# Optimization experiments

Hardware: AMD Instinct MI355X
Metric: run time of the kernel (lower is better)

## Reference

```python
import jax, jax.numpy as jnp
import numpy as np

N_NODES = 50000
N_EDGES = 800000
IN_DIM = 64
H_DIM = 64


def setup_inputs() -> dict:
    key = jax.random.key(0)
    ks = jax.random.split(key, 6)
    feat = jax.random.normal(ks[0], (N_NODES, IN_DIM), dtype=jnp.float32)
    W1 = jax.random.normal(ks[1], (IN_DIM, H_DIM), dtype=jnp.float32) * (1.0 / np.sqrt(IN_DIM))
    b1 = jnp.zeros((H_DIM,), dtype=jnp.float32)
    W2 = jax.random.normal(ks[2], (H_DIM, 1), dtype=jnp.float32) * (1.0 / np.sqrt(H_DIM))
    b2 = jnp.zeros((1,), dtype=jnp.float32)
    src = jax.random.randint(ks[3], (N_EDGES,), 0, N_NODES, dtype=jnp.int32)
    dst = jax.random.randint(ks[4], (N_EDGES,), 0, N_NODES, dtype=jnp.int32)
    return {"feat": feat, "W1": W1, "b1": b1, "W2": W2, "b2": b2, "src": src, "dst": dst}


def _norms(src, dst, n_nodes):
    # DGL GraphConv norm='both': symmetric D^{-1/2} A D^{-1/2}, degrees clamped to >=1
    ones = jnp.ones(src.shape[0], dtype=jnp.float32)
    out_deg = jax.ops.segment_sum(ones, src, num_segments=n_nodes)
    in_deg = jax.ops.segment_sum(ones, dst, num_segments=n_nodes)
    out_norm = jax.lax.rsqrt(jnp.clip(out_deg, 1.0))
    in_norm = jax.lax.rsqrt(jnp.clip(in_deg, 1.0))
    return out_norm, in_norm


def _graph_conv(feat, W, b, src, dst, out_norm, in_norm, act):
    h = feat * out_norm[:, None]          # scale source features by D_out^{-1/2}
    msg = h[src]                          # gather along edges [E, d]
    agg = jax.ops.segment_sum(msg, dst, num_segments=feat.shape[0])  # scatter-sum to dst
    agg = agg * in_norm[:, None]          # scale by D_in^{-1/2}
    return act(agg @ W + b)


def reference(feat, W1, b1, W2, b2, src, dst):
    out_norm, in_norm = _norms(src, dst, feat.shape[0])
    h = _graph_conv(feat, W1, b1, src, dst, out_norm, in_norm, jax.nn.relu)
    return _graph_conv(h, W2, b2, src, dst, out_norm, in_norm, jax.nn.sigmoid)
```

## Files before the change

kernel.cpp:

```cpp
#include <hip/hip_runtime.h>
#include <hip/hip_fp16.h>
#include <math.h>


#define BS 256
#define EPB 2048
#define SCB 2048

__global__ __launch_bounds__(256, 4)
void histA_featw1_kernel(const int* __restrict__ src, const int* __restrict__ dst,
                         const float* __restrict__ feat, const float* __restrict__ W1,
                         int* __restrict__ dhist,
                         __half* __restrict__ featp,
                         int E, int N, int NB, int T, int M) {
    __shared__ float4 ftile[64 * 16];
    __shared__ int histD[256];
    __shared__ int histS[256];
    int tid = threadIdx.x;
    if ((int)blockIdx.x < T) {
        histD[tid] = 0; histS[tid] = 0;
        __syncthreads();
        int base = blockIdx.x * EPB;
        #pragma unroll
        for (int it = 0; it < EPB / BS; it++) {
            int e = base + it * BS + tid;
            if (e < E) {
                atomicAdd(&histD[dst[e] >> 8], 1);
                atomicAdd(&histS[src[e] >> 8], 1);
            }
        }
        __syncthreads();
        if (tid < NB) {
            dhist[tid * T + (int)blockIdx.x] = histD[tid];
            dhist[M + tid * T + (int)blockIdx.x] = histS[tid];
        }
    } else {
        int lane = tid & 63;
        int wave = tid >> 6;
        #define WD(i) float wv##i = W1[(i) * 64 + lane];
        WD(0)  WD(1)  WD(2)  WD(3)  WD(4)  WD(5)  WD(6)  WD(7)
        WD(8)  WD(9)  WD(10) WD(11) WD(12) WD(13) WD(14) WD(15)
        WD(16) WD(17) WD(18) WD(19) WD(20) WD(21) WD(22) WD(23)
        WD(24) WD(25) WD(26) WD(27) WD(28) WD(29) WD(30) WD(31)
        WD(32) WD(33) WD(34) WD(35) WD(36) WD(37) WD(38) WD(39)
        WD(40) WD(41) WD(42) WD(43) WD(44) WD(45) WD(46) WD(47)
        WD(48) WD(49) WD(50) WD(51) WD(52) WD(53) WD(54) WD(55)
        WD(56) WD(57) WD(58) WD(59) WD(60) WD(61) WD(62) WD(63)
        #undef WD
        int rBase = ((int)blockIdx.x - T) * 64;
        const float4* feat4 = (const float4*)feat;
        int maxF4 = N * 16 - 1;
        #pragma unroll
        for (int it = 0; it < 4; it++) {
            int idx = it * BS + tid;
            ftile[idx] = feat4[min(rBase * 16 + idx, maxF4)];
        }
        __syncthreads();
        #pragma unroll 1
        for (int rr = 0; rr < 16; rr++) {
            int r = wave * 16 + rr;
            const float4* ft = &ftile[r * 16];
            float a0 = 0.0f, a1 = 0.0f, a2 = 0.0f, a3 = 0.0f;
            #define RK(k4, wA, wB, wC, wD_) { float4 f = ft[k4]; \
                a0 = fmaf(f.x, wA, a0); a1 = fmaf(f.y, wB, a1); \
                a2 = fmaf(f.z, wC, a2); a3 = fmaf(f.w, wD_, a3); }
            RK(0,  wv0,  wv1,  wv2,  wv3)  RK(1,  wv4,  wv5,  wv6,  wv7)
            RK(2,  wv8,  wv9,  wv10, wv11) RK(3,  wv12, wv13, wv14, wv15)
            RK(4,  wv16, wv17, wv18, wv19) RK(5,  wv20, wv21, wv22, wv23)
            RK(6,  wv24, wv25, wv26, wv27) RK(7,  wv28, wv29, wv30, wv31)
            RK(8,  wv32, wv33, wv34, wv35) RK(9,  wv36, wv37, wv38, wv39)
            RK(10, wv40, wv41, wv42, wv43) RK(11, wv44, wv45, wv46, wv47)
            RK(12, wv48, wv49, wv50, wv51) RK(13, wv52, wv53, wv54, wv55)
            RK(14, wv56, wv57, wv58, wv59) RK(15, wv60, wv61, wv62, wv63)
            #undef RK
            int rowg = rBase + r;
            if (rowg < N)
                featp[(size_t)rowg * 64 + lane] = __float2half((a0 + a1) + (a2 + a3));
        }
    }
}

__global__ void scan1_kernel(const int* __restrict__ dhist, int* __restrict__ bsum, int M2) {
    __shared__ int s[256];
    int t = threadIdx.x;
    int base = blockIdx.x * SCB + t * 8;
    int sum = 0;
    #pragma unroll
    for (int i = 0; i < 8; i++) {
        int k = base + i;
        if (k < M2) sum += dhist[k];
    }
    s[t] = sum; __syncthreads();
    for (int off = 1; off < 256; off <<= 1) {
        int u = (t >= off) ? s[t - off] : 0; __syncthreads();
        s[t] += u; __syncthreads();
    }
    if (t == 255) bsum[blockIdx.x] = s[255];
}

__global__ void scan2_kernel(int* __restrict__ bsum, int NSB) {
    __shared__ int s[256];
    int t = threadIdx.x;
    int v = (t < NSB) ? bsum[t] : 0;
    s[t] = v; __syncthreads();
    for (int off = 1; off < 256; off <<= 1) {
        int u = (t >= off) ? s[t - off] : 0; __syncthreads();
        s[t] += u; __syncthreads();
    }
    if (t < NSB) bsum[t] = s[t] - v;
}

__global__ void scan3_kernel(int* __restrict__ dhist, const int* __restrict__ bsum, int M2) {
    __shared__ int s[256];
    int t = threadIdx.x;
    int base = blockIdx.x * SCB + t * 8;
    int v[8];
    int sum = 0;
    #pragma unroll
    for (int i = 0; i < 8; i++) {
        int k = base + i;
        v[i] = (k < M2) ? dhist[k] : 0;
        sum += v[i];
    }
    s[t] = sum; __syncthreads();
    for (int off = 1; off < 256; off <<= 1) {
        int u = (t >= off) ? s[t - off] : 0; __syncthreads();
        s[t] += u; __syncthreads();
    }
    int run = bsum[blockIdx.x] + s[t] - sum;
    #pragma unroll
    for (int i = 0; i < 8; i++) {
        int k = base + i;
        if (k < M2) dhist[k] = run;
        run += v[i];
    }
}

__global__ void partition_kernel(const int* __restrict__ src, const int* __restrict__ dst,
                                 const int* __restrict__ dhist,
                                 int* __restrict__ packed, unsigned char* __restrict__ srcPartB,
                                 int E, int NB, int T, int M) {
    __shared__ int darr[256];
    __shared__ int sarr[256];
    int tid = threadIdx.x;
    int b = blockIdx.x;
    darr[tid] = (tid < NB) ? dhist[tid * T + b] : 0;
    sarr[tid] = (tid < NB) ? (dhist[M + tid * T + b] - E) : 0;
    __syncthreads();
    int base = b * EPB;
    #pragma unroll
    for (int it = 0; it < EPB / BS; it++) {
        int e = base + it * BS + tid;
        if (e < E) {
            int d = dst[e], s2 = src[e];
            int pos = atomicAdd(&darr[d >> 8], 1);
            packed[pos] = s2 | ((d & 255) << 17);
            int pos2 = atomicAdd(&sarr[s2 >> 8], 1);
            srcPartB[pos2] = (unsigned char)(s2 & 255);
        }
    }
}

__global__ void finalize_kernel(const int* __restrict__ dhist,
                                const int* __restrict__ packed,
                                const unsigned char* __restrict__ srcPartB,
                                int* __restrict__ csr_src, int* __restrict__ in_deg,
                                int* __restrict__ row_start, int* __restrict__ out_deg,
                                __half* __restrict__ featp,
                                int N, int NB, int T, int M, int E) {
    __shared__ int hist[256];
    __shared__ int sc[256];
    int tid = threadIdx.x;
    int b = blockIdx.x;
    if (b < NB) {
        int lo = dhist[b * T];
        int hi = (b + 1 < NB) ? dhist[(b + 1) * T] : E;
        hist[tid] = 0; __syncthreads();
        for (int i = lo + tid; i < hi; i += BS)
            atomicAdd(&hist[(packed[i] >> 17) & 255], 1);
        __syncthreads();
        int v = hist[tid];
        sc[tid] = v; __syncthreads();
        for (int off = 1; off < 256; off <<= 1) {
            int u = (tid >= off) ? sc[tid - off] : 0; __syncthreads();
            sc[tid] += u; __syncthreads();
        }
        int ex = sc[tid] - v;
        int n = b * 256 + tid;
        if (n < N) { in_deg[n] = v; row_start[n] = lo + ex; }
        sc[tid] = lo + ex;
        __syncthreads();
        for (int i = lo + tid; i < hi; i += BS) {
            int pv = packed[i];
            int pos = atomicAdd(&sc[(pv >> 17) & 255], 1);
            csr_src[pos] = pv & 0x1FFFF;
        }
    } else {
        int sb = b - NB;
        int lo = dhist[M + sb * T] - E;
        int hi = ((sb + 1 < NB) ? dhist[M + (sb + 1) * T] : 2 * E) - E;
        hist[tid] = 0; __syncthreads();
        for (int i = lo + tid; i < hi; i += BS)
            atomicAdd(&hist[srcPartB[i]], 1);
        __syncthreads();
        int n = sb * 256 + tid;
        int od = hist[tid];
        if (n < N) out_deg[n] = od;
        float* snorm = (float*)sc;
        snorm[tid] = rsqrtf(fmaxf((float)od, 1.0f));
        __syncthreads();
        int nodes = min(256, N - sb * 256);
        uint4* fp = (uint4*)(featp + (size_t)sb * 256 * 64);
        int total = nodes * 8;
        for (int i = tid; i < total; i += BS) {
            float s = snorm[i >> 3];
            uint4 u = fp[i];
            __half2* hh = (__half2*)&u;
            #pragma unroll
            for (int c = 0; c < 4; c++) {
                float2 p = __half22float2(hh[c]);
                p.x *= s; p.y *= s;
                hh[c] = __float22half2_rn(p);
            }
            fp[i] = u;
        }
    }
}

__global__ void csr_agg1_kernel(const int* __restrict__ row_start, const int* __restrict__ in_deg,
                                const int* __restrict__ csr_src, const int* __restrict__ out_deg,
                                const __half* __restrict__ featp,
                                const float* __restrict__ b1, const float* __restrict__ W2,
                                float* __restrict__ s_buf, int N) {
    int gid = blockIdx.x * blockDim.x + threadIdx.x;
    int n = gid >> 6;
    if (n >= N) return;
    int lane = threadIdx.x & 63;
    int g = lane >> 3;
    int l = lane & 7;
    int start = row_start[n];
    int deg = in_deg[n];
    float acc[8] = {0, 0, 0, 0, 0, 0, 0, 0};
    const uint4* fp4 = (const uint4*)featp;
    for (int j = 0; j < deg; j += 16) {
        int e0 = j + g;
        int e1 = j + 8 + g;
        bool p0 = e0 < deg;
        bool p1 = e1 < deg;
        int sn0 = p0 ? csr_src[start + e0] : 0;
        int sn1 = p1 ? csr_src[start + e1] : 0;
        uint4 q0 = {0, 0, 0, 0}, q1 = {0, 0, 0, 0};
        if (p0) q0 = fp4[(size_t)sn0 * 8 + l];
        if (p1) q1 = fp4[(size_t)sn1 * 8 + l];
        const __half2* h0 = (const __half2*)&q0;
        const __half2* h1 = (const __half2*)&q1;
        #pragma unroll
        for (int c = 0; c < 4; c++) {
            float2 f0 = __half22float2(h0[c]);
            float2 f1 = __half22float2(h1[c]);
            acc[2 * c]     += f0.x + f1.x;
            acc[2 * c + 1] += f0.y + f1.y;
        }
    }
    #pragma unroll
    for (int off = 8; off < 64; off <<= 1) {
        #pragma unroll
        for (int c = 0; c < 8; c++)
            acc[c] += __shfl_xor(acc[c], off, 64);
    }
    float inn = rsqrtf(fmaxf((float)deg, 1.0f));
    float v = 0.0f;
    #pragma unroll
    for (int c = 0; c < 8; c++) {
        float h = fmaxf(inn * acc[c] + b1[l * 8 + c], 0.0f);
        v += h * W2[l * 8 + c];
    }
    #pragma unroll
    for (int off = 1; off < 8; off <<= 1)
        v += __shfl_xor(v, off, 64);
    if (lane == 0)
        s_buf[n] = rsqrtf(fmaxf((float)out_deg[n], 1.0f)) * v;
}

__global__ void csr_agg2_kernel(const int* __restrict__ row_start, const int* __restrict__ in_deg,
                                const int* __restrict__ csr_src,
                                const float* __restrict__ s_buf, const float* __restrict__ b2,
                                float* __restrict__ out, int N) {
    int gid = blockIdx.x * blockDim.x + threadIdx.x;
    int n = gid >> 4;
    if (n >= N) return;
    int sub = gid & 15;
    int start = row_start[n];
    int deg = in_deg[n];
    float a = 0.0f;
    for (int j = sub; j < deg; j += 32) {
        int j1 = j + 16;
        int i0 = csr_src[start + j];
        int i1 = (j1 < deg) ? csr_src[start + j1] : 0;
        float v0 = s_buf[i0];
        float v1 = (j1 < deg) ? s_buf[i1] : 0.0f;
        a += v0 + v1;
    }
    #pragma unroll
    for (int off = 1; off < 16; off <<= 1)
        a += __shfl_xor(a, off, 64);
    if (sub == 0) {
        float x = rsqrtf(fmaxf((float)deg, 1.0f)) * a + b2[0];
        out[n] = 1.0f / (1.0f + expf(-x));
    }
}

extern "C" void kernel_launch(void* const* d_in, const int* in_sizes, int n_in,
                              void* d_out, int out_size, void* d_ws, size_t ws_size,
                              hipStream_t stream) {
    const float* feat = (const float*)d_in[0];
    const float* W1   = (const float*)d_in[1];
    const float* b1   = (const float*)d_in[2];
    const float* W2   = (const float*)d_in[3];
    const float* b2   = (const float*)d_in[4];
    const int* src = (const int*)d_in[5];
    const int* dst = (const int*)d_in[6];
    float* out = (float*)d_out;

    const int N  = in_sizes[0] / 64;
    const int E  = in_sizes[5];
    const int NB = (N + 255) >> 8;
    const int T  = (E + EPB - 1) / EPB;
    const int M  = NB * T;
    const int M2 = 2 * M;
    const int NSB = (M2 + SCB - 1) / SCB;

    int* wsi = (int*)d_ws;
    int* bsum        = wsi;
    int* in_deg      = bsum + NSB;
    int* row_start   = in_deg + N;
    int* out_deg     = row_start + N;
    int* dhist       = out_deg + N;
    int* packed      = dhist + M2;
    int* csr_src     = packed + E;
    unsigned char* srcPartB = (unsigned char*)(csr_src + E);
    size_t int_bytes = ((size_t)NSB + 3 * (size_t)N + (size_t)M2 + 2 * (size_t)E) * sizeof(int)
                     + (size_t)E;
    size_t half_off  = (int_bytes + 15) & ~(size_t)15;
    __half* featp = (__half*)((char*)d_ws + half_off);
    float* s_buf  = (float*)((char*)d_ws + half_off + (size_t)64 * N * sizeof(__half));

    histA_featw1_kernel<<<T + (N + 63) / 64, BS, 0, stream>>>(
        src, dst, feat, W1, dhist, featp, E, N, NB, T, M);
    scan1_kernel<<<NSB, 256, 0, stream>>>(dhist, bsum, M2);
    scan2_kernel<<<1, 256, 0, stream>>>(bsum, NSB);
    scan3_kernel<<<NSB, 256, 0, stream>>>(dhist, bsum, M2);
    partition_kernel<<<T, BS, 0, stream>>>(src, dst, dhist, packed, srcPartB, E, NB, T, M);
    finalize_kernel<<<2 * NB, BS, 0, stream>>>(
        dhist, packed, srcPartB, csr_src, in_deg, row_start, out_deg, featp, N, NB, T, M, E);
    csr_agg1_kernel<<<(int)(((size_t)N * 64 + BS - 1) / BS), BS, 0, stream>>>(
        row_start, in_deg, csr_src, out_deg, featp, b1, W2, s_buf, N);
    csr_agg2_kernel<<<(int)(((size_t)N * 16 + BS - 1) / BS), BS, 0, stream>>>(
        row_start, in_deg, csr_src, s_buf, b2, out, N);
}
```

Before: 158.5 us.

## Fuse all pipeline stages into one cooperative persistent kernel with grid syncs

Merges the eight separate launches (histogram+feature transform, three scan passes, partition, finalize, two aggregation passes) into a single cooperative kernel. Stages are separated by grid-wide barriers, and blocks loop over virtual block indices. The goal is to remove per-launch overhead and inter-kernel gaps. In exchange it depends on cooperative launch with an occupancy-limited grid, which may cut parallelism in the aggregation stages. Grid barriers also have their own cost, and the 256-register-heavy feature stage limits occupancy for every stage.

```diff
diff --git a/kernel.cpp b/kernel.cpp
--- a/kernel.cpp
+++ b/kernel.cpp
@@ -1,6 +1,9 @@
 #include <hip/hip_runtime.h>
 #include <hip/hip_fp16.h>
+#include <hip/hip_cooperative_groups.h>
 #include <math.h>
+
+namespace cg = cooperative_groups;
 
 
 #define BS 256
@@ -8,327 +11,311 @@
 #define SCB 2048
 
 __global__ __launch_bounds__(256, 4)
-void histA_featw1_kernel(const int* __restrict__ src, const int* __restrict__ dst,
-                         const float* __restrict__ feat, const float* __restrict__ W1,
-                         int* __restrict__ dhist,
-                         __half* __restrict__ featp,
-                         int E, int N, int NB, int T, int M) {
+void gcn_mega_kernel(const int* __restrict__ src, const int* __restrict__ dst,
+                     const float* __restrict__ feat, const float* __restrict__ W1,
+                     const float* __restrict__ b1, const float* __restrict__ W2,
+                     const float* __restrict__ b2,
+                     int* __restrict__ dhist, int* __restrict__ bsum,
+                     int* __restrict__ in_deg, int* __restrict__ row_start,
+                     int* __restrict__ out_deg, int* __restrict__ packed,
+                     unsigned char* __restrict__ srcPartB, int* __restrict__ csr_src,
+                     __half* __restrict__ featp, float* __restrict__ s_buf,
+                     float* __restrict__ out,
+                     int E, int N, int NB, int T, int M, int NSB, int NF, int NA1, int NA2)
+{
+    cg::grid_group grid = cg::this_grid();
     __shared__ float4 ftile[64 * 16];
-    __shared__ int histD[256];
-    __shared__ int histS[256];
-    int tid = threadIdx.x;
-    if ((int)blockIdx.x < T) {
-        histD[tid] = 0; histS[tid] = 0;
+    __shared__ int shA[256];
+    __shared__ int shB[256];
+    const int tid = threadIdx.x;
+    const int nblk = gridDim.x;
+    const int M2 = 2 * M;
+
+    for (int vb = blockIdx.x; vb < T + NF; vb += nblk) {
+        if (vb < T) {
+            shA[tid] = 0; shB[tid] = 0;
+            __syncthreads();
+            int base = vb * EPB;
+            #pragma unroll
+            for (int it = 0; it < EPB / BS; it++) {
+                int e = base + it * BS + tid;
+                if (e < E) {
+                    atomicAdd(&shA[dst[e] >> 8], 1);
+                    atomicAdd(&shB[src[e] >> 8], 1);
+                }
+            }
+            __syncthreads();
+            if (tid < NB) {
+                dhist[tid * T + vb] = shA[tid];
+                dhist[M + tid * T + vb] = shB[tid];
+            }
+            __syncthreads();
+        } else {
+            int lane = tid & 63, wave = tid >> 6;
+            #define WD(i) float wv##i = W1[(i) * 64 + lane];
+            WD(0)  WD(1)  WD(2)  WD(3)  WD(4)  WD(5)  WD(6)  WD(7)
+            WD(8)  WD(9)  WD(10) WD(11) WD(12) WD(13) WD(14) WD(15)
+            WD(16) WD(17) WD(18) WD(19) WD(20) WD(21) WD(22) WD(23)
+            WD(24) WD(25) WD(26) WD(27) WD(28) WD(29) WD(30) WD(31)
+            WD(32) WD(33) WD(34) WD(35) WD(36) WD(37) WD(38) WD(39)
+            WD(40) WD(41) WD(42) WD(43) WD(44) WD(45) WD(46) WD(47)
+            WD(48) WD(49) WD(50) WD(51) WD(52) WD(53) WD(54) WD(55)
+            WD(56) WD(57) WD(58) WD(59) WD(60) WD(61) WD(62) WD(63)
+            #undef WD
+            int rBase = (vb - T) * 64;
+            const float4* feat4 = (const float4*)feat;
+            int maxF4 = N * 16 - 1;
+            #pragma unroll
+            for (int it = 0; it < 4; it++) {
+                int idx = it * BS + tid;
+                ftile[idx] = feat4[min(rBase * 16 + idx, maxF4)];
+            }
+            __syncthreads();
+            #pragma unroll 1
+            for (int rr = 0; rr < 16; rr++) {
+                int r = wave * 16 + rr;
+                const float4* ft = &ftile[r * 16];
+                float a0 = 0.0f, a1 = 0.0f, a2 = 0.0f, a3 = 0.0f;
+                #define RK(k4, wA, wB, wC, wD_) { float4 f = ft[k4]; \
+                    a0 = fmaf(f.x, wA, a0); a1 = fmaf(f.y, wB, a1); \
+                    a2 = fmaf(f.z, wC, a2); a3 = fmaf(f.w, wD_, a3); }
+                RK(0,  wv0,  wv1,  wv2,  wv3)  RK(1,  wv4,  wv5,  wv6,  wv7)
+                RK(2,  wv8,  wv9,  wv10, wv11) RK(3,  wv12, wv13, wv14, wv15)
+                RK(4,  wv16, wv17, wv18, wv19) RK(5,  wv20, wv21, wv22, wv23)
+                RK(6,  wv24, wv25, wv26, wv27) RK(7,  wv28, wv29, wv30, wv31)
+                RK(8,  wv32, wv33, wv34, wv35) RK(9,  wv36, wv37, wv38, wv39)
+                RK(10, wv40, wv41, wv42, wv43) RK(11, wv44, wv45, wv46, wv47)
+                RK(12, wv48, wv49, wv50, wv51) RK(13, wv52, wv53, wv54, wv55)
+                RK(14, wv56, wv57, wv58, wv59) RK(15, wv60, wv61, wv62, wv63)
+                #undef RK
+                int rowg = rBase + r;
+                if (rowg < N)
+                    featp[(size_t)rowg * 64 + lane] = __float2half((a0 + a1) + (a2 + a3));
+            }
+            __syncthreads();
+        }
+    }
+    grid.sync();
+
+    for (int vb = blockIdx.x; vb < NSB; vb += nblk) {
+        int base = vb * SCB + tid * 8;
+        int sum = 0;
+        #pragma unroll
+        for (int i = 0; i < 8; i++) { int k = base + i; if (k < M2) sum += dhist[k]; }
+        shA[tid] = sum; __syncthreads();
+        for (int off = 1; off < 256; off <<= 1) {
+            int u = (tid >= off) ? shA[tid - off] : 0; __syncthreads();
+            shA[tid] += u; __syncthreads();
+        }
+        if (tid == 255) bsum[vb] = shA[255];
         __syncthreads();
-        int base = blockIdx.x * EPB;
+    }
+    grid.sync();
+
+    for (int vb = blockIdx.x; vb < NSB; vb += nblk) {
+        int v0 = (tid < NSB) ? bsum[tid] : 0;
+        shA[tid] = v0; __syncthreads();
+        for (int off = 1; off < 256; off <<= 1) {
+            int u = (tid >= off) ? shA[tid - off] : 0; __syncthreads();
+            shA[tid] += u; __syncthreads();
+        }
+        int blkBase = (vb > 0) ? shA[vb - 1] : 0;
+        int base = vb * SCB + tid * 8;
+        int v[8]; int sum = 0;
+        #pragma unroll
+        for (int i = 0; i < 8; i++) { int k = base + i; v[i] = (k < M2) ? dhist[k] : 0; sum += v[i]; }
+        shB[tid] = sum; __syncthreads();
+        for (int off = 1; off < 256; off <<= 1) {
+            int u = (tid >= off) ? shB[tid - off] : 0; __syncthreads();
+            shB[tid] += u; __syncthreads();
+        }
+        int run = blkBase + shB[tid] - sum;
+        #pragma unroll
+        for (int i = 0; i < 8; i++) { int k = base + i; if (k < M2) dhist[k] = run; run += v[i]; }
+        __syncthreads();
+    }
+    grid.sync();
+
+    for (int vb = blockIdx.x; vb < T; vb += nblk) {
+        shA[tid] = (tid < NB) ? dhist[tid * T + vb] : 0;
+        shB[tid] = (tid < NB) ? (dhist[M + tid * T + vb] - E) : 0;
+        __syncthreads();
+        int base = vb * EPB;
         #pragma unroll
         for (int it = 0; it < EPB / BS; it++) {
             int e = base + it * BS + tid;
             if (e < E) {
-                atomicAdd(&histD[dst[e] >> 8], 1);
-                atomicAdd(&histS[src[e] >> 8], 1);
+                int d = dst[e], s2 = src[e];
+                int pos = atomicAdd(&shA[d >> 8], 1);
+                packed[pos] = s2 | ((d & 255) << 17);
+                int pos2 = atomicAdd(&shB[s2 >> 8], 1);
+                srcPartB[pos2] = (unsigned char)(s2 & 255);
             }
         }
         __syncthreads();
-        if (tid < NB) {
-            dhist[tid * T + (int)blockIdx.x] = histD[tid];
-            dhist[M + tid * T + (int)blockIdx.x] = histS[tid];
-        }
-    } else {
-        int lane = tid & 63;
-        int wave = tid >> 6;
-        #define WD(i) float wv##i = W1[(i) * 64 + lane];
-        WD(0)  WD(1)  WD(2)  WD(3)  WD(4)  WD(5)  WD(6)  WD(7)
-        WD(8)  WD(9)  WD(10) WD(11) WD(12) WD(13) WD(14) WD(15)
-        WD(16) WD(17) WD(18) WD(19) WD(20) WD(21) WD(22) WD(23)
-        WD(24) WD(25) WD(26) WD(27) WD(28) WD(29) WD(30) WD(31)
-        WD(32) WD(33) WD(34) WD(35) WD(36) WD(37) WD(38) WD(39)
-        WD(40) WD(41) WD(42) WD(43) WD(44) WD(45) WD(46) WD(47)
-        WD(48) WD(49) WD(50) WD(51) WD(52) WD(53) WD(54) WD(55)
-        WD(56) WD(57) WD(58) WD(59) WD(60) WD(61) WD(62) WD(63)
-        #undef WD
-        int rBase = ((int)blockIdx.x - T) * 64;
-        const float4* feat4 = (const float4*)feat;
-        int maxF4 = N * 16 - 1;
-        #pragma unroll
-        for (int it = 0; it < 4; it++) {
-            int idx = it * BS + tid;
-            ftile[idx] = feat4[min(rBase * 16 + idx, maxF4)];
-        }
-        __syncthreads();
-        #pragma unroll 1
-        for (int rr = 0; rr < 16; rr++) {
-            int r = wave * 16 + rr;
-            const float4* ft = &ftile[r * 16];
-            float a0 = 0.0f, a1 = 0.0f, a2 = 0.0f, a3 = 0.0f;
-            #define RK(k4, wA, wB, wC, wD_) { float4 f = ft[k4]; \
-                a0 = fmaf(f.x, wA, a0); a1 = fmaf(f.y, wB, a1); \
-                a2 = fmaf(f.z, wC, a2); a3 = fmaf(f.w, wD_, a3); }
-            RK(0,  wv0,  wv1,  wv2,  wv3)  RK(1,  wv4,  wv5,  wv6,  wv7)
-            RK(2,  wv8,  wv9,  wv10, wv11) RK(3,  wv12, wv13, wv14, wv15)
-            RK(4,  wv16, wv17, wv18, wv19) RK(5,  wv20, wv21, wv22, wv23)
-            RK(6,  wv24, wv25, wv26, wv27) RK(7,  wv28, wv29, wv30, wv31)
-            RK(8,  wv32, wv33, wv34, wv35) RK(9,  wv36, wv37, wv38, wv39)
-            RK(10, wv40, wv41, wv42, wv43) RK(11, wv44, wv45, wv46, wv47)
-            RK(12, wv48, wv49, wv50, wv51) RK(13, wv52, wv53, wv54, wv55)
-            RK(14, wv56, wv57, wv58, wv59) RK(15, wv60, wv61, wv62, wv63)
-            #undef RK
-            int rowg = rBase + r;
-            if (rowg < N)
-                featp[(size_t)rowg * 64 + lane] = __float2half((a0 + a1) + (a2 + a3));
-        }
-    }
-}
-
-__global__ void scan1_kernel(const int* __restrict__ dhist, int* __restrict__ bsum, int M2) {
-    __shared__ int s[256];
-    int t = threadIdx.x;
-    int base = blockIdx.x * SCB + t * 8;
-    int sum = 0;
-    #pragma unroll
-    for (int i = 0; i < 8; i++) {
-        int k = base + i;
-        if (k < M2) sum += dhist[k];
-    }
-    s[t] = sum; __syncthreads();
-    for (int off = 1; off < 256; off <<= 1) {
-        int u = (t >= off) ? s[t - off] : 0; __syncthreads();
-        s[t] += u; __syncthreads();
-    }
-    if (t == 255) bsum[blockIdx.x] = s[255];
-}
-
-__global__ void scan2_kernel(int* __restrict__ bsum, int NSB) {
-    __shared__ int s[256];
-    int t = threadIdx.x;
-    int v = (t < NSB) ? bsum[t] : 0;
-    s[t] = v; __syncthreads();
-    for (int off = 1; off < 256; off <<= 1) {
-        int u = (t >= off) ? s[t - off] : 0; __syncthreads();
-        s[t] += u; __syncthreads();
-    }
-    if (t < NSB) bsum[t] = s[t] - v;
-}
-
-__global__ void scan3_kernel(int* __restrict__ dhist, const int* __restrict__ bsum, int M2) {
-    __shared__ int s[256];
-    int t = threadIdx.x;
-    int base = blockIdx.x * SCB + t * 8;
-    int v[8];
-    int sum = 0;
-    #pragma unroll
-    for (int i = 0; i < 8; i++) {
-        int k = base + i;
-        v[i] = (k < M2) ? dhist[k] : 0;
-        sum += v[i];
-    }
-    s[t] = sum; __syncthreads();
-    for (int off = 1; off < 256; off <<= 1) {
-        int u = (t >= off) ? s[t - off] : 0; __syncthreads();
-        s[t] += u; __syncthreads();
-    }
-    int run = bsum[blockIdx.x] + s[t] - sum;
-    #pragma unroll
-    for (int i = 0; i < 8; i++) {
-        int k = base + i;
-        if (k < M2) dhist[k] = run;
-        run += v[i];
-    }
-}
-
-__global__ void partition_kernel(const int* __restrict__ src, const int* __restrict__ dst,
-                                 const int* __restrict__ dhist,
-                                 int* __restrict__ packed, unsigned char* __restrict__ srcPartB,
-                                 int E, int NB, int T, int M) {
-    __shared__ int darr[256];
-    __shared__ int sarr[256];
-    int tid = threadIdx.x;
-    int b = blockIdx.x;
-    darr[tid] = (tid < NB) ? dhist[tid * T + b] : 0;
-    sarr[tid] = (tid < NB) ? (dhist[M + tid * T + b] - E) : 0;
-    __syncthreads();
-    int base = b * EPB;
-    #pragma unroll
-    for (int it = 0; it < EPB / BS; it++) {
-        int e = base + it * BS + tid;
-        if (e < E) {
-            int d = dst[e], s2 = src[e];
-            int pos = atomicAdd(&darr[d >> 8], 1);
-            packed[pos] = s2 | ((d & 255) << 17);
-            int pos2 = atomicAdd(&sarr[s2 >> 8], 1);
-            srcPartB[pos2] = (unsigned char)(s2 & 255);
-        }
-    }
-}
-
-__global__ void finalize_kernel(const int* __restrict__ dhist,
-                                const int* __restrict__ packed,
-                                const unsigned char* __restrict__ srcPartB,
-                                int* __restrict__ csr_src, int* __restrict__ in_deg,
-                                int* __restrict__ row_start, int* __restrict__ out_deg,
-                                __half* __restrict__ featp,
-                                int N, int NB, int T, int M, int E) {
-    __shared__ int hist[256];
-    __shared__ int sc[256];
-    int tid = threadIdx.x;
-    int b = blockIdx.x;
-    if (b < NB) {
-        int lo = dhist[b * T];
-        int hi = (b + 1 < NB) ? dhist[(b + 1) * T] : E;
-        hist[tid] = 0; __syncthreads();
-        for (int i = lo + tid; i < hi; i += BS)
-            atomicAdd(&hist[(packed[i] >> 17) & 255], 1);
-        __syncthreads();
-        int v = hist[tid];
-        sc[tid] = v; __syncthreads();
-        for (int off = 1; off < 256; off <<= 1) {
-            int u = (tid >= off) ? sc[tid - off] : 0; __syncthreads();
-            sc[tid] += u; __syncthreads();
-        }
-        int ex = sc[tid] - v;
-        int n = b * 256 + tid;
-        if (n < N) { in_deg[n] = v; row_start[n] = lo + ex; }
-        sc[tid] = lo + ex;
-        __syncthreads();
-        for (int i = lo + tid; i < hi; i += BS) {
-            int pv = packed[i];
-            int pos = atomicAdd(&sc[(pv >> 17) & 255], 1);
-            csr_src[pos] = pv & 0x1FFFF;
-        }
-    } else {
-        int sb = b - NB;
-        int lo = dhist[M + sb * T] - E;
-        int hi = ((sb + 1 < NB) ? dhist[M + (sb + 1) * T] : 2 * E) - E;
-        hist[tid] = 0; __syncthreads();
-        for (int i = lo + tid; i < hi; i += BS)
-            atomicAdd(&hist[srcPartB[i]], 1);
-        __syncthreads();
-        int n = sb * 256 + tid;
-        int od = hist[tid];
-        if (n < N) out_deg[n] = od;
-        float* snorm = (float*)sc;
-        snorm[tid] = rsqrtf(fmaxf((float)od, 1.0f));
-        __syncthreads();
-        int nodes = min(256, N - sb * 256);
-        uint4* fp = (uint4*)(featp + (size_t)sb * 256 * 64);
-        int total = nodes * 8;
-        for (int i = tid; i < total; i += BS) {
-            float s = snorm[i >> 3];
-            uint4 u = fp[i];
-            __half2* hh = (__half2*)&u;
-            #pragma unroll
-            for (int c = 0; c < 4; c++) {
-                float2 p = __half22float2(hh[c]);
-                p.x *= s; p.y *= s;
-                hh[c] = __float22half2_rn(p);
-            }
-            fp[i] = u;
-        }
-    }
-}
-
-__global__ void csr_agg1_kernel(const int* __restrict__ row_start, const int* __restrict__ in_deg,
-                                const int* __restrict__ csr_src, const int* __restrict__ out_deg,
-                                const __half* __restrict__ featp,
-                                const float* __restrict__ b1, const float* __restrict__ W2,
-                                float* __restrict__ s_buf, int N) {
-    int gid = blockIdx.x * blockDim.x + threadIdx.x;
-    int n = gid >> 6;
-    if (n >= N) return;
-    int lane = threadIdx.x & 63;
-    int g = lane >> 3;
-    int l = lane & 7;
-    int start = row_start[n];
-    int deg = in_deg[n];
-    float acc[8] = {0, 0, 0, 0, 0, 0, 0, 0};
-    const uint4* fp4 = (const uint4*)featp;
-    for (int j = 0; j < deg; j += 16) {
-        int e0 = j + g;
-        int e1 = j + 8 + g;
-        bool p0 = e0 < deg;
-        bool p1 = e1 < deg;
-        int sn0 = p0 ? csr_src[start + e0] : 0;
-        int sn1 = p1 ? csr_src[start + e1] : 0;
-        uint4 q0 = {0, 0, 0, 0}, q1 = {0, 0, 0, 0};
-        if (p0) q0 = fp4[(size_t)sn0 * 8 + l];
-        if (p1) q1 = fp4[(size_t)sn1 * 8 + l];
-        const __half2* h0 = (const __half2*)&q0;
-        const __half2* h1 = (const __half2*)&q1;
-        #pragma unroll
-        for (int c = 0; c < 4; c++) {
-            float2 f0 = __half22float2(h0[c]);
-            float2 f1 = __half22float2(h1[c]);
-            acc[2 * c]     += f0.x + f1.x;
-            acc[2 * c + 1] += f0.y + f1.y;
-        }
-    }
-    #pragma unroll
-    for (int off = 8; off < 64; off <<= 1) {
-        #pragma unroll
-        for (int c = 0; c < 8; c++)
-            acc[c] += __shfl_xor(acc[c], off, 64);
-    }
-    float inn = rsqrtf(fmaxf((float)deg, 1.0f));
-    float v = 0.0f;
-    #pragma unroll
-    for (int c = 0; c < 8; c++) {
-        float h = fmaxf(inn * acc[c] + b1[l * 8 + c], 0.0f);
-        v += h * W2[l * 8 + c];
-    }
-    #pragma unroll
-    for (int off = 1; off < 8; off <<= 1)
-        v += __shfl_xor(v, off, 64);
-    if (lane == 0)
-        s_buf[n] = rsqrtf(fmaxf((float)out_deg[n], 1.0f)) * v;
-}
-
-__global__ void csr_agg2_kernel(const int* __restrict__ row_start, const int* __restrict__ in_deg,
-                                const int* __restrict__ csr_src,
-                                const float* __restrict__ s_buf, const float* __restrict__ b2,
-                                float* __restrict__ out, int N) {
-    int gid = blockIdx.x * blockDim.x + threadIdx.x;
-    int n = gid >> 4;
-    if (n >= N) return;
-    int sub = gid & 15;
-    int start = row_start[n];
-    int deg = in_deg[n];
-    float a = 0.0f;
-    for (int j = sub; j < deg; j += 32) {
-        int j1 = j + 16;
-        int i0 = csr_src[start + j];
-        int i1 = (j1 < deg) ? csr_src[start + j1] : 0;
-        float v0 = s_buf[i0];
-        float v1 = (j1 < deg) ? s_buf[i1] : 0.0f;
-        a += v0 + v1;
-    }
-    #pragma unroll
-    for (int off = 1; off < 16; off <<= 1)
-        a += __shfl_xor(a, off, 64);
-    if (sub == 0) {
-        float x = rsqrtf(fmaxf((float)deg, 1.0f)) * a + b2[0];
-        out[n] = 1.0f / (1.0f + expf(-x));
+    }
+    grid.sync();
+
+    for (int vb = blockIdx.x; vb < 2 * NB; vb += nblk) {
+        if (vb < NB) {
+            int b = vb;
+            int lo = dhist[b * T];
+            int hi = (b + 1 < NB) ? dhist[(b + 1) * T] : E;
+            shA[tid] = 0; __syncthreads();
+            for (int i = lo + tid; i < hi; i += BS)
+                atomicAdd(&shA[(packed[i] >> 17) & 255], 1);
+            __syncthreads();
+            int v = shA[tid];
+            shB[tid] = v; __syncthreads();
+            for (int off = 1; off < 256; off <<= 1) {
+                int u = (tid >= off) ? shB[tid - off] : 0; __syncthreads();
+                shB[tid] += u; __syncthreads();
+            }
+            int ex = shB[tid] - v;
+            int n = b * 256 + tid;
+            if (n < N) { in_deg[n] = v; row_start[n] = lo + ex; }
+            shB[tid] = lo + ex;
+            __syncthreads();
+            for (int i = lo + tid; i < hi; i += BS) {
+                int pv = packed[i];
+                int pos = atomicAdd(&shB[(pv >> 17) & 255], 1);
+                csr_src[pos] = pv & 0x1FFFF;
+            }
+            __syncthreads();
+        } else {
+            int sb = vb - NB;
+            int lo = dhist[M + sb * T] - E;
+            int hi = ((sb + 1 < NB) ? dhist[M + (sb + 1) * T] : 2 * E) - E;
+            shA[tid] = 0; __syncthreads();
+            for (int i = lo + tid; i < hi; i += BS)
+                atomicAdd(&shA[srcPartB[i]], 1);
+            __syncthreads();
+            int n = sb * 256 + tid;
+            int od = shA[tid];
+            if (n < N) out_deg[n] = od;
+            float* snorm = (float*)shB;
+            snorm[tid] = rsqrtf(fmaxf((float)od, 1.0f));
+            __syncthreads();
+            int nodes = min(256, N - sb * 256);
+            uint4* fp = (uint4*)(featp + (size_t)sb * 256 * 64);
+            int total = nodes * 8;
+            for (int i = tid; i < total; i += BS) {
+                float s = snorm[i >> 3];
+                uint4 u = fp[i];
+                __half2* hh = (__half2*)&u;
+                #pragma unroll
+                for (int c = 0; c < 4; c++) {
+                    float2 p = __half22float2(hh[c]);
+                    p.x *= s; p.y *= s;
+                    hh[c] = __float22half2_rn(p);
+                }
+                fp[i] = u;
+            }
+            __syncthreads();
+        }
+    }
+    grid.sync();
+
+    for (int vb = blockIdx.x; vb < NA1; vb += nblk) {
+        int n = vb * 4 + (tid >> 6);
+        if (n < N) {
+            int lane = tid & 63;
+            int g = lane >> 3;
+            int l = lane & 7;
+            int start = row_start[n];
+            int deg = in_deg[n];
+            float acc[8] = {0, 0, 0, 0, 0, 0, 0, 0};
+            const uint4* fp4 = (const uint4*)featp;
+            for (int j = 0; j < deg; j += 16) {
+                int e0 = j + g;
+                int e1 = j + 8 + g;
+                bool p0 = e0 < deg;
+                bool p1 = e1 < deg;
+                int sn0 = p0 ? csr_src[start + e0] : 0;
+                int sn1 = p1 ? csr_src[start + e1] : 0;
+                uint4 q0 = {0, 0, 0, 0}, q1 = {0, 0, 0, 0};
+                if (p0) q0 = fp4[(size_t)sn0 * 8 + l];
+                if (p1) q1 = fp4[(size_t)sn1 * 8 + l];
+                const __half2* h0 = (const __half2*)&q0;
+                const __half2* h1 = (const __half2*)&q1;
+                #pragma unroll
+                for (int c = 0; c < 4; c++) {
+                    float2 f0 = __half22float2(h0[c]);
+                    float2 f1 = __half22float2(h1[c]);
+                    acc[2 * c]     += f0.x + f1.x;
+                    acc[2 * c + 1] += f0.y + f1.y;
+                }
+            }
+            #pragma unroll
+            for (int off = 8; off < 64; off <<= 1) {
+                #pragma unroll
+                for (int c = 0; c < 8; c++)
+                    acc[c] += __shfl_xor(acc[c], off, 64);
+            }
+            float inn = rsqrtf(fmaxf((float)deg, 1.0f));
+            float v = 0.0f;
+            #pragma unroll
+            for (int c = 0; c < 8; c++) {
+                float h = fmaxf(inn * acc[c] + b1[l * 8 + c], 0.0f);
+                v += h * W2[l * 8 + c];
+            }
+            #pragma unroll
+            for (int off = 1; off < 8; off <<= 1)
+                v += __shfl_xor(v, off, 64);
+            if (lane == 0)
+                s_buf[n] = rsqrtf(fmaxf((float)out_deg[n], 1.0f)) * v;
+        }
+    }
+    grid.sync();
+
+    for (int vb = blockIdx.x; vb < NA2; vb += nblk) {
+        int n = vb * 16 + (tid >> 4);
+        if (n < N) {
+            int sub = tid & 15;
+            int start = row_start[n];
+            int deg = in_deg[n];
+            float a = 0.0f;
+            for (int j = sub; j < deg; j += 32) {
+                int j1 = j + 16;
+                int i0 = csr_src[start + j];
+                int i1 = (j1 < deg) ? csr_src[start + j1] : 0;
+                float v0 = s_buf[i0];
+                float v1 = (j1 < deg) ? s_buf[i1] : 0.0f;
+                a += v0 + v1;
+            }
+            #pragma unroll
+            for (int off = 1; off < 16; off <<= 1)
+                a += __shfl_xor(a, off, 64);
+            if (sub == 0) {
+                float x = rsqrtf(fmaxf((float)deg, 1.0f)) * a + b2[0];
+                out[n] = 1.0f / (1.0f + expf(-x));
+            }
+        }
     }
 }
 
 extern "C" void kernel_launch(void* const* d_in, const int* in_sizes, int n_in,
                               void* d_out, int out_size, void* d_ws, size_t ws_size,
                               hipStream_t stream) {
+    const int* src = (const int*)d_in[5];
+    const int* dst = (const int*)d_in[6];
     const float* feat = (const float*)d_in[0];
     const float* W1   = (const float*)d_in[1];
     const float* b1   = (const float*)d_in[2];
     const float* W2   = (const float*)d_in[3];
     const float* b2   = (const float*)d_in[4];
-    const int* src = (const int*)d_in[5];
-    const int* dst = (const int*)d_in[6];
     float* out = (float*)d_out;
 
-    const int N  = in_sizes[0] / 64;
-    const int E  = in_sizes[5];
-    const int NB = (N + 255) >> 8;
-    const int T  = (E + EPB - 1) / EPB;
-    const int M  = NB * T;
-    const int M2 = 2 * M;
-    const int NSB = (M2 + SCB - 1) / SCB;
+    int N  = in_sizes[0] / 64;
+    int E  = in_sizes[5];
+    int NB = (N + 255) >> 8;
+    int T  = (E + EPB - 1) / EPB;
+    int M  = NB * T;
+    int M2 = 2 * M;
+    int NSB = (M2 + SCB - 1) / SCB;
+    int NF  = (N + 63) / 64;
+    int NA1 = (N + 3) / 4;
+    int NA2 = (N + 15) / 16;
 
     int* wsi = (int*)d_ws;
     int* bsum        = wsi;
@@ -345,16 +332,28 @@
     __half* featp = (__half*)((char*)d_ws + half_off);
     float* s_buf  = (float*)((char*)d_ws + half_off + (size_t)64 * N * sizeof(__half));
 
-    histA_featw1_kernel<<<T + (N + 63) / 64, BS, 0, stream>>>(
-        src, dst, feat, W1, dhist, featp, E, N, NB, T, M);
-    scan1_kernel<<<NSB, 256, 0, stream>>>(dhist, bsum, M2);
-    scan2_kernel<<<1, 256, 0, stream>>>(bsum, NSB);
-    scan3_kernel<<<NSB, 256, 0, stream>>>(dhist, bsum, M2);
-    partition_kernel<<<T, BS, 0, stream>>>(src, dst, dhist, packed, srcPartB, E, NB, T, M);
-    finalize_kernel<<<2 * NB, BS, 0, stream>>>(
-        dhist, packed, srcPartB, csr_src, in_deg, row_start, out_deg, featp, N, NB, T, M, E);
-    csr_agg1_kernel<<<(int)(((size_t)N * 64 + BS - 1) / BS), BS, 0, stream>>>(
-        row_start, in_deg, csr_src, out_deg, featp, b1, W2, s_buf, N);
-    csr_agg2_kernel<<<(int)(((size_t)N * 16 + BS - 1) / BS), BS, 0, stream>>>(
-        row_start, in_deg, csr_src, s_buf, b2, out, N);
+    static int gridBlocks = 0;
+    if (gridBlocks == 0) {
+        int mb = 0;
+        hipOccupancyMaxActiveBlocksPerMultiprocessor(&mb, gcn_mega_kernel, BS, 0);
+        if (mb < 1) mb = 1;
+        int dev = 0;
+        hipGetDevice(&dev);
+        hipDeviceProp_t prop;
+        int cus = 256;
+        if (hipGetDeviceProperties(&prop, dev) == hipSuccess && prop.multiProcessorCount > 0)
+            cus = prop.multiProcessorCount;
+        gridBlocks = cus * mb;
+        if (gridBlocks > 2048) gridBlocks = 2048;
+    }
+
+    void* args[] = { (void*)&src, (void*)&dst, (void*)&feat, (void*)&W1,
+                     (void*)&b1, (void*)&W2, (void*)&b2,
+                     (void*)&dhist, (void*)&bsum, (void*)&in_deg, (void*)&row_start,
+                     (void*)&out_deg, (void*)&packed, (void*)&srcPartB, (void*)&csr_src,
+                     (void*)&featp, (void*)&s_buf, (void*)&out,
+                     (void*)&E, (void*)&N, (void*)&NB, (void*)&T, (void*)&M,
+                     (void*)&NSB, (void*)&NF, (void*)&NA1, (void*)&NA2 };
+    hipLaunchCooperativeKernel(gcn_mega_kernel, dim3(gridBlocks), dim3(BS),
+                               args, 0, stream);
 }
```

Result: slower. 620.1 us (+291.3%).

## Replace three-kernel histogram scan with last-block bin scan and atomic cursors

Applied to the files above, without the earlier changes.

The three scan kernels over the per-block histogram matrix are removed. Per-bin totals are now accumulated atomically in the histogram kernel, and the last block to finish, detected through a done counter, scans the bin totals. The partition kernel then claims offsets inside each bin with atomic cursors instead of reading precomputed exclusive prefixes. This drops two kernel launches and a pass over the histogram, but adds a memset, global atomics, and ordering inside each bin that is no longer deterministic.

```diff
diff --git a/kernel.cpp b/kernel.cpp
--- a/kernel.cpp
+++ b/kernel.cpp
@@ -5,17 +5,21 @@
 
 #define BS 256
 #define EPB 2048
-#define SCB 2048
 
 __global__ __launch_bounds__(256, 4)
 void histA_featw1_kernel(const int* __restrict__ src, const int* __restrict__ dst,
                          const float* __restrict__ feat, const float* __restrict__ W1,
                          int* __restrict__ dhist,
+                         int* __restrict__ binCountD, int* __restrict__ binCountS,
+                         int* __restrict__ doneCnt,
+                         int* __restrict__ dstBinBase, int* __restrict__ srcBinBase,
+                         int* __restrict__ dstCursor, int* __restrict__ srcCursor,
                          __half* __restrict__ featp,
                          int E, int N, int NB, int T, int M) {
     __shared__ float4 ftile[64 * 16];
     __shared__ int histD[256];
     __shared__ int histS[256];
+    __shared__ int isLast;
     int tid = threadIdx.x;
     if ((int)blockIdx.x < T) {
         histD[tid] = 0; histS[tid] = 0;
@@ -31,8 +35,11 @@
         }
         __syncthreads();
         if (tid < NB) {
-            dhist[tid * T + (int)blockIdx.x] = histD[tid];
-            dhist[M + tid * T + (int)blockIdx.x] = histS[tid];
+            int hd = histD[tid], hs = histS[tid];
+            dhist[tid * T + (int)blockIdx.x] = hd;
+            dhist[M + tid * T + (int)blockIdx.x] = hs;
+            if (hd) atomicAdd(&binCountD[tid], hd);
+            if (hs) atomicAdd(&binCountS[tid], hs);
         }
     } else {
         int lane = tid & 63;
@@ -78,74 +85,54 @@
                 featp[(size_t)rowg * 64 + lane] = __float2half((a0 + a1) + (a2 + a3));
         }
     }
-}
-
-__global__ void scan1_kernel(const int* __restrict__ dhist, int* __restrict__ bsum, int M2) {
-    __shared__ int s[256];
-    int t = threadIdx.x;
-    int base = blockIdx.x * SCB + t * 8;
-    int sum = 0;
-    #pragma unroll
-    for (int i = 0; i < 8; i++) {
-        int k = base + i;
-        if (k < M2) sum += dhist[k];
-    }
-    s[t] = sum; __syncthreads();
-    for (int off = 1; off < 256; off <<= 1) {
-        int u = (t >= off) ? s[t - off] : 0; __syncthreads();
-        s[t] += u; __syncthreads();
-    }
-    if (t == 255) bsum[blockIdx.x] = s[255];
-}
-
-__global__ void scan2_kernel(int* __restrict__ bsum, int NSB) {
-    __shared__ int s[256];
-    int t = threadIdx.x;
-    int v = (t < NSB) ? bsum[t] : 0;
-    s[t] = v; __syncthreads();
-    for (int off = 1; off < 256; off <<= 1) {
-        int u = (t >= off) ? s[t - off] : 0; __syncthreads();
-        s[t] += u; __syncthreads();
-    }
-    if (t < NSB) bsum[t] = s[t] - v;
-}
-
-__global__ void scan3_kernel(int* __restrict__ dhist, const int* __restrict__ bsum, int M2) {
-    __shared__ int s[256];
-    int t = threadIdx.x;
-    int base = blockIdx.x * SCB + t * 8;
-    int v[8];
-    int sum = 0;
-    #pragma unroll
-    for (int i = 0; i < 8; i++) {
-        int k = base + i;
-        v[i] = (k < M2) ? dhist[k] : 0;
-        sum += v[i];
-    }
-    s[t] = sum; __syncthreads();
-    for (int off = 1; off < 256; off <<= 1) {
-        int u = (t >= off) ? s[t - off] : 0; __syncthreads();
-        s[t] += u; __syncthreads();
-    }
-    int run = bsum[blockIdx.x] + s[t] - sum;
-    #pragma unroll
-    for (int i = 0; i < 8; i++) {
-        int k = base + i;
-        if (k < M2) dhist[k] = run;
-        run += v[i];
+    __syncthreads();
+    if (tid == 0) {
+        __threadfence();
+        int old = atomicAdd(doneCnt, 1);
+        isLast = (old == (int)gridDim.x - 1) ? 1 : 0;
+    }
+    __syncthreads();
+    if (isLast) {
+        __threadfence();
+        int v = (tid < NB) ? binCountD[tid] : 0;
+        histD[tid] = v; __syncthreads();
+        for (int off = 1; off < 256; off <<= 1) {
+            int u = (tid >= off) ? histD[tid - off] : 0; __syncthreads();
+            histD[tid] += u; __syncthreads();
+        }
+        if (tid < NB) {
+            int ex = histD[tid] - v;
+            dstBinBase[tid] = ex; dstCursor[tid] = ex;
+            if (tid == NB - 1) dstBinBase[NB] = histD[tid];
+        }
+        __syncthreads();
+        v = (tid < NB) ? binCountS[tid] : 0;
+        histD[tid] = v; __syncthreads();
+        for (int off = 1; off < 256; off <<= 1) {
+            int u = (tid >= off) ? histD[tid - off] : 0; __syncthreads();
+            histD[tid] += u; __syncthreads();
+        }
+        if (tid < NB) {
+            int ex = histD[tid] - v;
+            srcBinBase[tid] = ex; srcCursor[tid] = ex;
+            if (tid == NB - 1) srcBinBase[NB] = histD[tid];
+        }
     }
 }
 
 __global__ void partition_kernel(const int* __restrict__ src, const int* __restrict__ dst,
                                  const int* __restrict__ dhist,
+                                 int* __restrict__ dstCursor, int* __restrict__ srcCursor,
                                  int* __restrict__ packed, unsigned char* __restrict__ srcPartB,
                                  int E, int NB, int T, int M) {
     __shared__ int darr[256];
     __shared__ int sarr[256];
     int tid = threadIdx.x;
     int b = blockIdx.x;
-    darr[tid] = (tid < NB) ? dhist[tid * T + b] : 0;
-    sarr[tid] = (tid < NB) ? (dhist[M + tid * T + b] - E) : 0;
+    int hd = (tid < NB) ? dhist[tid * T + b] : 0;
+    int hs = (tid < NB) ? dhist[M + tid * T + b] : 0;
+    darr[tid] = (hd > 0) ? atomicAdd(&dstCursor[tid], hd) : 0;
+    sarr[tid] = (hs > 0) ? atomicAdd(&srcCursor[tid], hs) : 0;
     __syncthreads();
     int base = b * EPB;
     #pragma unroll
@@ -161,20 +148,19 @@
     }
 }
 
-__global__ void finalize_kernel(const int* __restrict__ dhist,
+__global__ void finalize_kernel(const int* __restrict__ dstBinBase, const int* __restrict__ srcBinBase,
                                 const int* __restrict__ packed,
                                 const unsigned char* __restrict__ srcPartB,
                                 int* __restrict__ csr_src, int* __restrict__ in_deg,
                                 int* __restrict__ row_start, int* __restrict__ out_deg,
                                 __half* __restrict__ featp,
-                                int N, int NB, int T, int M, int E) {
+                                int N, int NB) {
     __shared__ int hist[256];
     __shared__ int sc[256];
     int tid = threadIdx.x;
     int b = blockIdx.x;
     if (b < NB) {
-        int lo = dhist[b * T];
-        int hi = (b + 1 < NB) ? dhist[(b + 1) * T] : E;
+        int lo = dstBinBase[b], hi = dstBinBase[b + 1];
         hist[tid] = 0; __syncthreads();
         for (int i = lo + tid; i < hi; i += BS)
             atomicAdd(&hist[(packed[i] >> 17) & 255], 1);
@@ -197,8 +183,7 @@
         }
     } else {
         int sb = b - NB;
-        int lo = dhist[M + sb * T] - E;
-        int hi = ((sb + 1 < NB) ? dhist[M + (sb + 1) * T] : 2 * E) - E;
+        int lo = srcBinBase[sb], hi = srcBinBase[sb + 1];
         hist[tid] = 0; __syncthreads();
         for (int i = lo + tid; i < hi; i += BS)
             atomicAdd(&hist[srcPartB[i]], 1);
@@ -322,37 +307,43 @@
     const int* dst = (const int*)d_in[6];
     float* out = (float*)d_out;
 
-    const int N  = in_sizes[0] / 64;
-    const int E  = in_sizes[5];
-    const int NB = (N + 255) >> 8;
-    const int T  = (E + EPB - 1) / EPB;
-    const int M  = NB * T;
-    const int M2 = 2 * M;
-    const int NSB = (M2 + SCB - 1) / SCB;
+    int N  = in_sizes[0] / 64;
+    int E  = in_sizes[5];
+    int NB = (N + 255) >> 8;
+    int T  = (E + EPB - 1) / EPB;
+    int M  = NB * T;
 
     int* wsi = (int*)d_ws;
-    int* bsum        = wsi;
-    int* in_deg      = bsum + NSB;
+    int* binCountD   = wsi;
+    int* binCountS   = binCountD + NB;
+    int* doneCnt     = binCountS + NB;
+    int* dstBinBase  = doneCnt + 1;
+    int* srcBinBase  = dstBinBase + NB + 1;
+    int* dstCursor   = srcBinBase + NB + 1;
+    int* srcCursor   = dstCursor + NB;
+    int* in_deg      = srcCursor + NB;
     int* row_start   = in_deg + N;
     int* out_deg     = row_start + N;
     int* dhist       = out_deg + N;
-    int* packed      = dhist + M2;
+    int* packed      = dhist + 2 * M;
     int* csr_src     = packed + E;
     unsigned char* srcPartB = (unsigned char*)(csr_src + E);
-    size_t int_bytes = ((size_t)NSB + 3 * (size_t)N + (size_t)M2 + 2 * (size_t)E) * sizeof(int)
+    size_t int_bytes = ((size_t)(6 * NB + 3) + 3 * (size_t)N + 2 * (size_t)M + 2 * (size_t)E) * sizeof(int)
                      + (size_t)E;
     size_t half_off  = (int_bytes + 15) & ~(size_t)15;
     __half* featp = (__half*)((char*)d_ws + half_off);
     float* s_buf  = (float*)((char*)d_ws + half_off + (size_t)64 * N * sizeof(__half));
 
+    hipMemsetAsync(binCountD, 0, (size_t)(2 * NB + 1) * sizeof(int), stream);
+
     histA_featw1_kernel<<<T + (N + 63) / 64, BS, 0, stream>>>(
-        src, dst, feat, W1, dhist, featp, E, N, NB, T, M);
-    scan1_kernel<<<NSB, 256, 0, stream>>>(dhist, bsum, M2);
-    scan2_kernel<<<1, 256, 0, stream>>>(bsum, NSB);
-    scan3_kernel<<<NSB, 256, 0, stream>>>(dhist, bsum, M2);
-    partition_kernel<<<T, BS, 0, stream>>>(src, dst, dhist, packed, srcPartB, E, NB, T, M);
+        src, dst, feat, W1, dhist, binCountD, binCountS, doneCnt,
+        dstBinBase, srcBinBase, dstCursor, srcCursor, featp, E, N, NB, T, M);
+    partition_kernel<<<T, BS, 0, stream>>>(
+        src, dst, dhist, dstCursor, srcCursor, packed, srcPartB, E, NB, T, M);
     finalize_kernel<<<2 * NB, BS, 0, stream>>>(
-        dhist, packed, srcPartB, csr_src, in_deg, row_start, out_deg, featp, N, NB, T, M, E);
+        dstBinBase, srcBinBase, packed, srcPartB, csr_src, in_deg, row_start,
+        out_deg, featp, N, NB);
     csr_agg1_kernel<<<(int)(((size_t)N * 64 + BS - 1) / BS), BS, 0, stream>>>(
         row_start, in_deg, csr_src, out_deg, featp, b1, W2, s_buf, N);
     csr_agg2_kernel<<<(int)(((size_t)N * 16 + BS - 1) / BS), BS, 0, stream>>>(
```

Measured after the change: 206.7 us. 30.5% more time.
